# Performance work log

Measured on AMD Instinct MI355X. Metric: run time of the kernel, lower is better.

The kernel has to match this reference:

```python
import jax, jax.numpy as jnp
import numpy as np
import math

B, G, QLEN, KVLEN = 2, 2, 1024, 1024
DIN = 1024
NUM_HEADS = 16
QK_CH = 1024
V_CH = 1024
OUT_CH = 1024


def setup_inputs() -> dict:
    key = jax.random.key(0)
    ks = jax.random.split(key, 8)
    s_q = (1.0 / math.sqrt(DIN)) * math.sqrt(2.0)  # kaiming-ish scale
    inputs_q = jax.random.normal(ks[0], (B, G, QLEN, DIN), dtype=jnp.float32)
    inputs_kv = jax.random.normal(ks[1], (B, G, KVLEN, DIN), dtype=jnp.float32)
    Wq = jax.random.normal(ks[2], (QK_CH, DIN), dtype=jnp.float32) * s_q
    bq = jnp.zeros((QK_CH,), dtype=jnp.float32)
    Wk = jax.random.normal(ks[3], (QK_CH, DIN), dtype=jnp.float32) * s_q
    bk = jnp.zeros((QK_CH,), dtype=jnp.float32)
    Wv = jax.random.normal(ks[4], (V_CH, DIN), dtype=jnp.float32) * s_q
    bv = jnp.zeros((V_CH,), dtype=jnp.float32)
    Wo = jax.random.normal(ks[5], (OUT_CH, V_CH), dtype=jnp.float32) * (1.0 / math.sqrt(V_CH)) * math.sqrt(2.0)
    bo = jnp.zeros((OUT_CH,), dtype=jnp.float32)
    return {"inputs_q": inputs_q, "inputs_kv": inputs_kv,
            "Wq": Wq, "bq": bq, "Wk": Wk, "bk": bk,
            "Wv": Wv, "bv": bv, "Wo": Wo, "bo": bo}


def reference(inputs_q, inputs_kv, Wq, bq, Wk, bk, Wv, bv, Wo, bo):
    h = NUM_HEADS
    qk_per_head = QK_CH // h
    v_per_head = V_CH // h
    b, g, n, _ = inputs_q.shape
    m = inputs_kv.shape[2]
    # linear projections (torch Linear: x @ W.T + b)
    q = inputs_q @ Wq.T + bq          # [b,g,n,qk]
    k = inputs_kv @ Wk.T + bk         # [b,g,m,qk]
    v = inputs_kv @ Wv.T + bv         # [b,g,m,vc]
    q = q.reshape(b, g, n, h, qk_per_head)
    k = k.reshape(b, g, m, h, qk_per_head)
    v = v.reshape(b, g, m, h, v_per_head)
    scale = 1.0 / math.sqrt(qk_per_head)
    attn_scores = jnp.einsum('bgnhc,bgmhc->bghnm', q, k) * scale
    attn_probs = jax.nn.softmax(attn_scores, axis=-1)  # dropout_prob=0 -> identity
    result = jnp.einsum('bghnm,bgmhd->bgnhd', attn_probs, v)
    result = result.reshape(b, g, n, h * v_per_head)
    out = result @ Wo.T + bo
    return (out, attn_probs)
```

## Files before the change

kernel.cpp:

```cpp
#include <hip/hip_runtime.h>
#include <math.h>

#define DIN   1024
#define NH    16
#define HD    64
#define SEQ   1024
#define BG    4
#define MROWS (BG*SEQ)

typedef unsigned short u16;
typedef __attribute__((ext_vector_type(8))) short bf16x8;
typedef __attribute__((ext_vector_type(4))) float f32x4;

__device__ __forceinline__ u16 f2bf(float f) {
    unsigned u = __float_as_uint(f);
    u += 0x7fff + ((u >> 16) & 1);
    return (u16)(u >> 16);
}

__global__ __launch_bounds__(256)
void convert_bf(const float* __restrict__ a, u16* __restrict__ o)
{
    const size_t i = ((size_t)blockIdx.x * 256 + threadIdx.x) * 4;
    const float4 v = *(const float4*)(a + i);
    ushort4 r;
    r.x = f2bf(v.x); r.y = f2bf(v.y); r.z = f2bf(v.z); r.w = f2bf(v.w);
    *(ushort4*)(o + i) = r;
}

template<int OUT_BF16>
__global__ __launch_bounds__(256)
void gemm_bt(const u16* __restrict__ A, int lda,
             const u16* __restrict__ W, int ldw,
             const float* __restrict__ bias,
             void* __restrict__ Cout, int ldc, int K)
{
    __shared__ u16 As[128][40];
    __shared__ u16 Ws[128][40];
    const int tid = threadIdx.x;
    const int wave = tid >> 6, lane = tid & 63;
    const int wm = wave >> 1, wn = wave & 1;
    const int q = lane >> 4, c = lane & 15;
    const int row0 = blockIdx.y * 128, col0 = blockIdx.x * 128;
    const int rs = tid >> 2, kg = (tid & 3) * 8;

    f32x4 acc[4][4];
    #pragma unroll
    for (int i = 0; i < 4; i++)
        #pragma unroll
        for (int j = 0; j < 4; j++) acc[i][j] = (f32x4){0.f, 0.f, 0.f, 0.f};

    for (int k0 = 0; k0 < K; k0 += 32) {
        *(float4*)&As[rs][kg]      = *(const float4*)(A + (size_t)(row0 + rs) * lda + k0 + kg);
        *(float4*)&As[rs + 64][kg] = *(const float4*)(A + (size_t)(row0 + rs + 64) * lda + k0 + kg);
        *(float4*)&Ws[rs][kg]      = *(const float4*)(W + (size_t)(col0 + rs) * ldw + k0 + kg);
        *(float4*)&Ws[rs + 64][kg] = *(const float4*)(W + (size_t)(col0 + rs + 64) * ldw + k0 + kg);
        __syncthreads();
        bf16x8 af[4], bfr[4];
        #pragma unroll
        for (int i = 0; i < 4; i++) af[i]  = *(const bf16x8*)&As[wm * 64 + i * 16 + c][q * 8];
        #pragma unroll
        for (int j = 0; j < 4; j++) bfr[j] = *(const bf16x8*)&Ws[wn * 64 + j * 16 + c][q * 8];
        #pragma unroll
        for (int i = 0; i < 4; i++)
            #pragma unroll
            for (int j = 0; j < 4; j++)
                acc[i][j] = __builtin_amdgcn_mfma_f32_16x16x32_bf16(af[i], bfr[j], acc[i][j], 0, 0, 0);
        __syncthreads();
    }

    float bv[4];
    #pragma unroll
    for (int j = 0; j < 4; j++) bv[j] = bias[col0 + wn * 64 + j * 16 + c];
    #pragma unroll
    for (int i = 0; i < 4; i++)
        #pragma unroll
        for (int r = 0; r < 4; r++) {
            const size_t row = row0 + wm * 64 + i * 16 + q * 4 + r;
            #pragma unroll
            for (int j = 0; j < 4; j++) {
                const int col = col0 + wn * 64 + j * 16 + c;
                const float v = acc[i][j][r] + bv[j];
                if (OUT_BF16) ((u16*)Cout)[row * ldc + col] = f2bf(v);
                else          ((float*)Cout)[row * ldc + col] = v;
            }
        }
}

__global__ __launch_bounds__(256, 2)
void attn_fused(const u16* __restrict__ Qbf, const u16* __restrict__ Kbf,
                const u16* __restrict__ Vbf, float* __restrict__ P,
                u16* __restrict__ Rbf)
{
    __shared__ u16 Ps[4][128][40];
    __shared__ u16 Vs[4][64][40];
    __shared__ float red[128][2];

    const int tid = threadIdx.x;
    const int wave = tid >> 6, lane = tid & 63;
    const int wm = wave >> 1, wn = wave & 1;
    const int q = lane >> 4, c = lane & 15;

    const int lin = blockIdx.y * 8 + blockIdx.x;
    const int xcd = lin & 7, li = lin >> 3;
    const int bgh = (xcd << 3) | (li >> 3);
    const int n0  = (li & 7) * 128;

    const int bg = bgh >> 4, h = bgh & 15;
    const u16* Qh = Qbf + (size_t)bg * SEQ * DIN + h * HD;
    const u16* Kh = Kbf + (size_t)bg * SEQ * DIN + h * HD;
    const u16* Vh = Vbf + (size_t)bg * SEQ * DIN + h * HD;
    float* Ph = P + (size_t)bgh * SEQ * SEQ;

    bf16x8 qf[4][2];
    #pragma unroll
    for (int i = 0; i < 4; i++)
        #pragma unroll
        for (int ks = 0; ks < 2; ks++)
            qf[i][ks] = *(const bf16x8*)(Qh + (size_t)(n0 + wm * 64 + i * 16 + c) * DIN + ks * 32 + q * 8);

    float lsum[4][4];
    #pragma unroll
    for (int i = 0; i < 4; i++)
        #pragma unroll
        for (int r = 0; r < 4; r++) lsum[i][r] = 0.f;

    #pragma unroll 1
    for (int m0 = 0; m0 < SEQ; m0 += 128) {
        f32x4 acc[4][4];
        #pragma unroll
        for (int i = 0; i < 4; i++)
            #pragma unroll
            for (int j = 0; j < 4; j++) acc[i][j] = (f32x4){0.f, 0.f, 0.f, 0.f};
        #pragma unroll
        for (int ks = 0; ks < 2; ks++) {
            bf16x8 kf[4];
            #pragma unroll
            for (int j = 0; j < 4; j++)
                kf[j] = *(const bf16x8*)(Kh + (size_t)(m0 + wn * 64 + j * 16 + c) * DIN + ks * 32 + q * 8);
            #pragma unroll
            for (int i = 0; i < 4; i++)
                #pragma unroll
                for (int j = 0; j < 4; j++)
                    acc[i][j] = __builtin_amdgcn_mfma_f32_16x16x32_bf16(qf[i][ks], kf[j], acc[i][j], 0, 0, 0);
        }
        #pragma unroll
        for (int i = 0; i < 4; i++)
            #pragma unroll
            for (int r = 0; r < 4; r++) {
                #pragma unroll
                for (int j = 0; j < 4; j++)
                    lsum[i][r] += __expf(acc[i][j][r] * 0.125f);
            }
    }

    #pragma unroll
    for (int i = 0; i < 4; i++)
        #pragma unroll
        for (int r = 0; r < 4; r++) {
            float s = lsum[i][r];
            s += __shfl_xor(s, 1);
            s += __shfl_xor(s, 2);
            s += __shfl_xor(s, 4);
            s += __shfl_xor(s, 8);
            if (c == 0) red[wm * 64 + i * 16 + q * 4 + r][wn] = s;
        }
    __syncthreads();
    float invl[4][4];
    #pragma unroll
    for (int i = 0; i < 4; i++)
        #pragma unroll
        for (int r = 0; r < 4; r++) {
            const int rl = wm * 64 + i * 16 + q * 4 + r;
            invl[i][r] = 1.f / (red[rl][0] + red[rl][1]);
        }

    f32x4 oacc[4][2];
    #pragma unroll
    for (int i = 0; i < 4; i++) {
        oacc[i][0] = (f32x4){0.f, 0.f, 0.f, 0.f};
        oacc[i][1] = (f32x4){0.f, 0.f, 0.f, 0.f};
    }

    #pragma unroll 1
    for (int m0 = 0; m0 < SEQ; m0 += 128) {
        f32x4 acc[4][4];
        #pragma unroll
        for (int i = 0; i < 4; i++)
            #pragma unroll
            for (int j = 0; j < 4; j++) acc[i][j] = (f32x4){0.f, 0.f, 0.f, 0.f};
        #pragma unroll
        for (int ks = 0; ks < 2; ks++) {
            bf16x8 kf[4];
            #pragma unroll
            for (int j = 0; j < 4; j++)
                kf[j] = *(const bf16x8*)(Kh + (size_t)(m0 + wn * 64 + j * 16 + c) * DIN + ks * 32 + q * 8);
            #pragma unroll
            for (int i = 0; i < 4; i++)
                #pragma unroll
                for (int j = 0; j < 4; j++)
                    acc[i][j] = __builtin_amdgcn_mfma_f32_16x16x32_bf16(qf[i][ks], kf[j], acc[i][j], 0, 0, 0);
        }

        #pragma unroll
        for (int it = 0; it < 4; it++) {
            const int mv = it * 32 + (tid >> 3);
            const int dg = (tid & 7) * 8;
            const bf16x8 vv = *(const bf16x8*)(Vh + (size_t)(m0 + mv) * DIN + dg);
            const u16* vp = (const u16*)&vv;
            #pragma unroll
            for (int u = 0; u < 8; u++) Vs[it][dg + u][tid >> 3] = vp[u];
        }

        #pragma unroll
        for (int i = 0; i < 4; i++)
            #pragma unroll
            for (int j = 0; j < 4; j++) {
                const int ml = wn * 64 + j * 16 + c;
                const int mc = ml >> 5, mw = ml & 31;
                #pragma unroll
                for (int r = 0; r < 4; r++) {
                    const float p = __expf(acc[i][j][r] * 0.125f) * invl[i][r];
                    const int row = wm * 64 + i * 16 + q * 4 + r;
                    Ph[(size_t)(n0 + row) * SEQ + m0 + ml] = p;
                    Ps[mc][row][mw] = f2bf(p);
                }
            }
        __syncthreads();

        #pragma unroll
        for (int ks = 0; ks < 4; ks++) {
            bf16x8 pf[4], vf[2];
            #pragma unroll
            for (int i = 0; i < 4; i++) pf[i] = *(const bf16x8*)&Ps[ks][wm * 64 + i * 16 + c][q * 8];
            #pragma unroll
            for (int j = 0; j < 2; j++) vf[j] = *(const bf16x8*)&Vs[ks][wn * 32 + j * 16 + c][q * 8];
            #pragma unroll
            for (int i = 0; i < 4; i++)
                #pragma unroll
                for (int j = 0; j < 2; j++)
                    oacc[i][j] = __builtin_amdgcn_mfma_f32_16x16x32_bf16(pf[i], vf[j], oacc[i][j], 0, 0, 0);
        }
        __syncthreads();
    }

    #pragma unroll
    for (int i = 0; i < 4; i++)
        #pragma unroll
        for (int r = 0; r < 4; r++) {
            const size_t row = (size_t)bg * SEQ + n0 + wm * 64 + i * 16 + q * 4 + r;
            #pragma unroll
            for (int j = 0; j < 2; j++) {
                const int d = wn * 32 + j * 16 + c;
                Rbf[row * DIN + h * HD + d] = f2bf(oacc[i][j][r]);
            }
        }
}

extern "C" void kernel_launch(void* const* d_in, const int* in_sizes, int n_in,
                              void* d_out, int out_size, void* d_ws, size_t ws_size,
                              hipStream_t stream)
{
    const float* xq  = (const float*)d_in[0];
    const float* xkv = (const float*)d_in[1];
    const float* Wq  = (const float*)d_in[2];
    const float* bq  = (const float*)d_in[3];
    const float* Wk  = (const float*)d_in[4];
    const float* bk  = (const float*)d_in[5];
    const float* Wv  = (const float*)d_in[6];
    const float* bv  = (const float*)d_in[7];
    const float* Wo  = (const float*)d_in[8];
    const float* bo  = (const float*)d_in[9];

    float* out0 = (float*)d_out;
    float* out1 = out0 + (size_t)MROWS * DIN;

    u16* xq_bf  = (u16*)d_ws;
    u16* xkv_bf = xq_bf  + (size_t)MROWS * DIN;
    u16* Wq_bf  = xkv_bf + (size_t)MROWS * DIN;
    u16* Wk_bf  = Wq_bf  + (size_t)DIN * DIN;
    u16* Wv_bf  = Wk_bf  + (size_t)DIN * DIN;
    u16* Wo_bf  = Wv_bf  + (size_t)DIN * DIN;
    u16* Qbf    = Wo_bf  + (size_t)DIN * DIN;
    u16* Kbf    = Qbf    + (size_t)MROWS * DIN;
    u16* Vbf    = Kbf    + (size_t)MROWS * DIN;
    u16* Rbf    = Vbf    + (size_t)MROWS * DIN;

    const dim3 blk(256);

    convert_bf<<<dim3(4096), blk, 0, stream>>>(xq,  xq_bf);
    convert_bf<<<dim3(4096), blk, 0, stream>>>(xkv, xkv_bf);
    convert_bf<<<dim3(1024), blk, 0, stream>>>(Wq,  Wq_bf);
    convert_bf<<<dim3(1024), blk, 0, stream>>>(Wk,  Wk_bf);
    convert_bf<<<dim3(1024), blk, 0, stream>>>(Wv,  Wv_bf);
    convert_bf<<<dim3(1024), blk, 0, stream>>>(Wo,  Wo_bf);

    gemm_bt<1><<<dim3(8, 32), blk, 0, stream>>>(xq_bf,  DIN, Wq_bf, DIN, bq, Qbf, DIN, DIN);
    gemm_bt<1><<<dim3(8, 32), blk, 0, stream>>>(xkv_bf, DIN, Wk_bf, DIN, bk, Kbf, DIN, DIN);
    gemm_bt<1><<<dim3(8, 32), blk, 0, stream>>>(xkv_bf, DIN, Wv_bf, DIN, bv, Vbf, DIN, DIN);

    attn_fused<<<dim3(8, 64), blk, 0, stream>>>(Qbf, Kbf, Vbf, out1, Rbf);

    gemm_bt<0><<<dim3(8, 32), blk, 0, stream>>>(Rbf, DIN, Wo_bf, DIN, bo, out0, DIN, DIN);
}
```

Before: 483.2 us.

## Fuse fp32-to-bf16 conversion into GEMM loads and produce transposed V directly

Drops the six separate fp32-to-bf16 conversion kernels. The GEMMs now read fp32 inputs and weights directly and convert them while staging into LDS. The V projection is computed as Wv·xkvᵀ so it writes V already transposed, with a row-wise bias. The attention kernel then reads V fragments straight from global memory, with no LDS transpose, and processes the score tile in two halves to lower register pressure, so occupancy can be raised to 3 blocks. The cost is that the GEMMs move twice the input bytes as fp32 and re-convert tiles they load more than once, and the V reads in the PV step become uncached global loads.

```diff
diff --git a/kernel.cpp b/kernel.cpp
--- a/kernel.cpp
+++ b/kernel.cpp
@@ -18,20 +18,26 @@
     return (u16)(u >> 16);
 }
 
+template<int FP32>
+__device__ __forceinline__ void stage8(u16* dst, const void* __restrict__ src, size_t off)
+{
+    if (FP32) {
+        const float* p = (const float*)src + off;
+        const float4 a = *(const float4*)p;
+        const float4 b = *(const float4*)(p + 4);
+        ushort4 r0, r1;
+        r0.x = f2bf(a.x); r0.y = f2bf(a.y); r0.z = f2bf(a.z); r0.w = f2bf(a.w);
+        r1.x = f2bf(b.x); r1.y = f2bf(b.y); r1.z = f2bf(b.z); r1.w = f2bf(b.w);
+        *(ushort4*)dst = r0; *(ushort4*)(dst + 4) = r1;
+    } else {
+        *(float4*)dst = *(const float4*)((const u16*)src + off);
+    }
+}
+
+template<int A_FP32, int W_FP32, int OUT_BF16, int BIAS_ROW>
 __global__ __launch_bounds__(256)
-void convert_bf(const float* __restrict__ a, u16* __restrict__ o)
-{
-    const size_t i = ((size_t)blockIdx.x * 256 + threadIdx.x) * 4;
-    const float4 v = *(const float4*)(a + i);
-    ushort4 r;
-    r.x = f2bf(v.x); r.y = f2bf(v.y); r.z = f2bf(v.z); r.w = f2bf(v.w);
-    *(ushort4*)(o + i) = r;
-}
-
-template<int OUT_BF16>
-__global__ __launch_bounds__(256)
-void gemm_bt(const u16* __restrict__ A, int lda,
-             const u16* __restrict__ W, int ldw,
+void gemm_bt(const void* __restrict__ A, int lda,
+             const void* __restrict__ W, int ldw,
              const float* __restrict__ bias,
              void* __restrict__ Cout, int ldc, int K)
 {
@@ -51,10 +57,10 @@
         for (int j = 0; j < 4; j++) acc[i][j] = (f32x4){0.f, 0.f, 0.f, 0.f};
 
     for (int k0 = 0; k0 < K; k0 += 32) {
-        *(float4*)&As[rs][kg]      = *(const float4*)(A + (size_t)(row0 + rs) * lda + k0 + kg);
-        *(float4*)&As[rs + 64][kg] = *(const float4*)(A + (size_t)(row0 + rs + 64) * lda + k0 + kg);
-        *(float4*)&Ws[rs][kg]      = *(const float4*)(W + (size_t)(col0 + rs) * ldw + k0 + kg);
-        *(float4*)&Ws[rs + 64][kg] = *(const float4*)(W + (size_t)(col0 + rs + 64) * ldw + k0 + kg);
+        stage8<A_FP32>(&As[rs][kg],      A, (size_t)(row0 + rs) * lda + k0 + kg);
+        stage8<A_FP32>(&As[rs + 64][kg], A, (size_t)(row0 + rs + 64) * lda + k0 + kg);
+        stage8<W_FP32>(&Ws[rs][kg],      W, (size_t)(col0 + rs) * ldw + k0 + kg);
+        stage8<W_FP32>(&Ws[rs + 64][kg], W, (size_t)(col0 + rs + 64) * ldw + k0 + kg);
         __syncthreads();
         bf16x8 af[4], bfr[4];
         #pragma unroll
@@ -69,9 +75,16 @@
         __syncthreads();
     }
 
-    float bv[4];
-    #pragma unroll
-    for (int j = 0; j < 4; j++) bv[j] = bias[col0 + wn * 64 + j * 16 + c];
+    float bcol[4], brow[4][4];
+    if (!BIAS_ROW) {
+        #pragma unroll
+        for (int j = 0; j < 4; j++) bcol[j] = bias[col0 + wn * 64 + j * 16 + c];
+    } else {
+        #pragma unroll
+        for (int i = 0; i < 4; i++)
+            #pragma unroll
+            for (int r = 0; r < 4; r++) brow[i][r] = bias[row0 + wm * 64 + i * 16 + q * 4 + r];
+    }
     #pragma unroll
     for (int i = 0; i < 4; i++)
         #pragma unroll
@@ -80,20 +93,19 @@
             #pragma unroll
             for (int j = 0; j < 4; j++) {
                 const int col = col0 + wn * 64 + j * 16 + c;
-                const float v = acc[i][j][r] + bv[j];
+                const float v = acc[i][j][r] + (BIAS_ROW ? brow[i][r] : bcol[j]);
                 if (OUT_BF16) ((u16*)Cout)[row * ldc + col] = f2bf(v);
                 else          ((float*)Cout)[row * ldc + col] = v;
             }
         }
 }
 
-__global__ __launch_bounds__(256, 2)
+__global__ __launch_bounds__(256, 3)
 void attn_fused(const u16* __restrict__ Qbf, const u16* __restrict__ Kbf,
-                const u16* __restrict__ Vbf, float* __restrict__ P,
+                const u16* __restrict__ Vt, float* __restrict__ P,
                 u16* __restrict__ Rbf)
 {
-    __shared__ u16 Ps[4][128][40];
-    __shared__ u16 Vs[4][64][40];
+    __shared__ u16 Ps[4][128][36];
     __shared__ float red[128][2];
 
     const int tid = threadIdx.x;
@@ -109,7 +121,7 @@
     const int bg = bgh >> 4, h = bgh & 15;
     const u16* Qh = Qbf + (size_t)bg * SEQ * DIN + h * HD;
     const u16* Kh = Kbf + (size_t)bg * SEQ * DIN + h * HD;
-    const u16* Vh = Vbf + (size_t)bg * SEQ * DIN + h * HD;
+    const u16* Vh = Vt  + (size_t)(h * HD) * MROWS + bg * SEQ;
     float* Ph = P + (size_t)bgh * SEQ * SEQ;
 
     bf16x8 qf[4][2];
@@ -184,48 +196,39 @@
 
     #pragma unroll 1
     for (int m0 = 0; m0 < SEQ; m0 += 128) {
-        f32x4 acc[4][4];
-        #pragma unroll
-        for (int i = 0; i < 4; i++)
-            #pragma unroll
-            for (int j = 0; j < 4; j++) acc[i][j] = (f32x4){0.f, 0.f, 0.f, 0.f};
-        #pragma unroll
-        for (int ks = 0; ks < 2; ks++) {
-            bf16x8 kf[4];
-            #pragma unroll
-            for (int j = 0; j < 4; j++)
-                kf[j] = *(const bf16x8*)(Kh + (size_t)(m0 + wn * 64 + j * 16 + c) * DIN + ks * 32 + q * 8);
+        #pragma unroll 1
+        for (int half = 0; half < 2; half++) {
+            f32x4 acc[4][2];
+            #pragma unroll
+            for (int i = 0; i < 4; i++) { acc[i][0] = (f32x4){0.f,0.f,0.f,0.f}; acc[i][1] = (f32x4){0.f,0.f,0.f,0.f}; }
+            #pragma unroll
+            for (int ks = 0; ks < 2; ks++) {
+                bf16x8 kf[2];
+                #pragma unroll
+                for (int j = 0; j < 2; j++)
+                    kf[j] = *(const bf16x8*)(Kh + (size_t)(m0 + wn * 64 + half * 32 + j * 16 + c) * DIN + ks * 32 + q * 8);
+                #pragma unroll
+                for (int i = 0; i < 4; i++)
+                    #pragma unroll
+                    for (int j = 0; j < 2; j++)
+                        acc[i][j] = __builtin_amdgcn_mfma_f32_16x16x32_bf16(qf[i][ks], kf[j], acc[i][j], 0, 0, 0);
+            }
+            const int mc = wn * 2 + half;
             #pragma unroll
             for (int i = 0; i < 4; i++)
                 #pragma unroll
-                for (int j = 0; j < 4; j++)
-                    acc[i][j] = __builtin_amdgcn_mfma_f32_16x16x32_bf16(qf[i][ks], kf[j], acc[i][j], 0, 0, 0);
-        }
-
-        #pragma unroll
-        for (int it = 0; it < 4; it++) {
-            const int mv = it * 32 + (tid >> 3);
-            const int dg = (tid & 7) * 8;
-            const bf16x8 vv = *(const bf16x8*)(Vh + (size_t)(m0 + mv) * DIN + dg);
-            const u16* vp = (const u16*)&vv;
-            #pragma unroll
-            for (int u = 0; u < 8; u++) Vs[it][dg + u][tid >> 3] = vp[u];
-        }
-
-        #pragma unroll
-        for (int i = 0; i < 4; i++)
-            #pragma unroll
-            for (int j = 0; j < 4; j++) {
-                const int ml = wn * 64 + j * 16 + c;
-                const int mc = ml >> 5, mw = ml & 31;
-                #pragma unroll
-                for (int r = 0; r < 4; r++) {
-                    const float p = __expf(acc[i][j][r] * 0.125f) * invl[i][r];
-                    const int row = wm * 64 + i * 16 + q * 4 + r;
-                    Ph[(size_t)(n0 + row) * SEQ + m0 + ml] = p;
-                    Ps[mc][row][mw] = f2bf(p);
+                for (int j = 0; j < 2; j++) {
+                    const int mw = j * 16 + c;
+                    const int ml = wn * 64 + half * 32 + mw;
+                    #pragma unroll
+                    for (int r = 0; r < 4; r++) {
+                        const float p = __expf(acc[i][j][r] * 0.125f) * invl[i][r];
+                        const int row = wm * 64 + i * 16 + q * 4 + r;
+                        Ph[(size_t)(n0 + row) * SEQ + m0 + ml] = p;
+                        Ps[mc][row][mw] = f2bf(p);
+                    }
                 }
-            }
+        }
         __syncthreads();
 
         #pragma unroll
@@ -234,7 +237,8 @@
             #pragma unroll
             for (int i = 0; i < 4; i++) pf[i] = *(const bf16x8*)&Ps[ks][wm * 64 + i * 16 + c][q * 8];
             #pragma unroll
-            for (int j = 0; j < 2; j++) vf[j] = *(const bf16x8*)&Vs[ks][wn * 32 + j * 16 + c][q * 8];
+            for (int j = 0; j < 2; j++)
+                vf[j] = *(const bf16x8*)(Vh + (size_t)(wn * 32 + j * 16 + c) * MROWS + m0 + ks * 32 + q * 8);
             #pragma unroll
             for (int i = 0; i < 4; i++)
                 #pragma unroll
@@ -275,31 +279,18 @@
     float* out0 = (float*)d_out;
     float* out1 = out0 + (size_t)MROWS * DIN;
 
-    u16* xq_bf  = (u16*)d_ws;
-    u16* xkv_bf = xq_bf  + (size_t)MROWS * DIN;
-    u16* Wq_bf  = xkv_bf + (size_t)MROWS * DIN;
-    u16* Wk_bf  = Wq_bf  + (size_t)DIN * DIN;
-    u16* Wv_bf  = Wk_bf  + (size_t)DIN * DIN;
-    u16* Wo_bf  = Wv_bf  + (size_t)DIN * DIN;
-    u16* Qbf    = Wo_bf  + (size_t)DIN * DIN;
-    u16* Kbf    = Qbf    + (size_t)MROWS * DIN;
-    u16* Vbf    = Kbf    + (size_t)MROWS * DIN;
-    u16* Rbf    = Vbf    + (size_t)MROWS * DIN;
+    u16* Qbf = (u16*)d_ws;
+    u16* Kbf = Qbf + (size_t)MROWS * DIN;
+    u16* Vt  = Kbf + (size_t)MROWS * DIN;
+    u16* Rbf = Vt  + (size_t)DIN * MROWS;
 
     const dim3 blk(256);
 
-    convert_bf<<<dim3(4096), blk, 0, stream>>>(xq,  xq_bf);
-    convert_bf<<<dim3(4096), blk, 0, stream>>>(xkv, xkv_bf);
-    convert_bf<<<dim3(1024), blk, 0, stream>>>(Wq,  Wq_bf);
-    convert_bf<<<dim3(1024), blk, 0, stream>>>(Wk,  Wk_bf);
-    convert_bf<<<dim3(1024), blk, 0, stream>>>(Wv,  Wv_bf);
-    convert_bf<<<dim3(1024), blk, 0, stream>>>(Wo,  Wo_bf);
-
-    gemm_bt<1><<<dim3(8, 32), blk, 0, stream>>>(xq_bf,  DIN, Wq_bf, DIN, bq, Qbf, DIN, DIN);
-    gemm_bt<1><<<dim3(8, 32), blk, 0, stream>>>(xkv_bf, DIN, Wk_bf, DIN, bk, Kbf, DIN, DIN);
-    gemm_bt<1><<<dim3(8, 32), blk, 0, stream>>>(xkv_bf, DIN, Wv_bf, DIN, bv, Vbf, DIN, DIN);
-
-    attn_fused<<<dim3(8, 64), blk, 0, stream>>>(Qbf, Kbf, Vbf, out1, Rbf);
-
-    gemm_bt<0><<<dim3(8, 32), blk, 0, stream>>>(Rbf, DIN, Wo_bf, DIN, bo, out0, DIN, DIN);
-}
+    gemm_bt<1,1,1,0><<<dim3(8, 32), blk, 0, stream>>>(xq,  DIN, Wq,  DIN, bq, Qbf, DIN, DIN);
+    gemm_bt<1,1,1,0><<<dim3(8, 32), blk, 0, stream>>>(xkv, DIN, Wk,  DIN, bk, Kbf, DIN, DIN);
+    gemm_bt<1,1,1,1><<<dim3(32, 8), blk, 0, stream>>>(Wv,  DIN, xkv, DIN, bv, Vt, MROWS, DIN);
+
+    attn_fused<<<dim3(8, 64), blk, 0, stream>>>(Qbf, Kbf, Vt, out1, Rbf);
+
+    gemm_bt<0,1,0,0><<<dim3(8, 32), blk, 0, stream>>>(Rbf, DIN, Wo, DIN, bo, out0, DIN, DIN);
+}
```

New measurement: 571.5 us. 1.18x slower.

## Transpose QK^T MFMA operands so probability stores become row-contiguous vectors

Applied to the files above, without the earlier changes.

The attention kernel now computes S^T by passing K fragments as the A operand and Q fragments as B. Each lane then holds four consecutive key columns for one query row, so the fp32 probability matrix can be written with 16-byte vector stores and the bf16 P tile in LDS with 8-byte stores, instead of scattered scalar writes. The row-sum reduction changes to cross-quad shuffles, and the LDS padding for Ps and Vs is shrunk. The new padding strides may create LDS bank conflicts on the transposed V writes or the P reads.

```diff
diff --git a/kernel.cpp b/kernel.cpp
--- a/kernel.cpp
+++ b/kernel.cpp
@@ -92,8 +92,8 @@
                 const u16* __restrict__ Vbf, float* __restrict__ P,
                 u16* __restrict__ Rbf)
 {
-    __shared__ u16 Ps[4][128][40];
-    __shared__ u16 Vs[4][64][40];
+    __shared__ u16 Ps[4][128][36];
+    __shared__ u16 Vs[4][64][34];
     __shared__ float red[128][2];
 
     const int tid = threadIdx.x;
@@ -114,66 +114,57 @@
 
     bf16x8 qf[4][2];
     #pragma unroll
-    for (int i = 0; i < 4; i++)
+    for (int jn = 0; jn < 4; jn++)
         #pragma unroll
         for (int ks = 0; ks < 2; ks++)
-            qf[i][ks] = *(const bf16x8*)(Qh + (size_t)(n0 + wm * 64 + i * 16 + c) * DIN + ks * 32 + q * 8);
-
-    float lsum[4][4];
-    #pragma unroll
-    for (int i = 0; i < 4; i++)
-        #pragma unroll
-        for (int r = 0; r < 4; r++) lsum[i][r] = 0.f;
+            qf[jn][ks] = *(const bf16x8*)(Qh + (size_t)(n0 + wm * 64 + jn * 16 + c) * DIN + ks * 32 + q * 8);
+
+    float lsum[4];
+    #pragma unroll
+    for (int jn = 0; jn < 4; jn++) lsum[jn] = 0.f;
 
     #pragma unroll 1
     for (int m0 = 0; m0 < SEQ; m0 += 128) {
         f32x4 acc[4][4];
         #pragma unroll
-        for (int i = 0; i < 4; i++)
-            #pragma unroll
-            for (int j = 0; j < 4; j++) acc[i][j] = (f32x4){0.f, 0.f, 0.f, 0.f};
+        for (int im = 0; im < 4; im++)
+            #pragma unroll
+            for (int jn = 0; jn < 4; jn++) acc[im][jn] = (f32x4){0.f, 0.f, 0.f, 0.f};
         #pragma unroll
         for (int ks = 0; ks < 2; ks++) {
             bf16x8 kf[4];
             #pragma unroll
-            for (int j = 0; j < 4; j++)
-                kf[j] = *(const bf16x8*)(Kh + (size_t)(m0 + wn * 64 + j * 16 + c) * DIN + ks * 32 + q * 8);
-            #pragma unroll
-            for (int i = 0; i < 4; i++)
-                #pragma unroll
-                for (int j = 0; j < 4; j++)
-                    acc[i][j] = __builtin_amdgcn_mfma_f32_16x16x32_bf16(qf[i][ks], kf[j], acc[i][j], 0, 0, 0);
-        }
-        #pragma unroll
-        for (int i = 0; i < 4; i++)
-            #pragma unroll
-            for (int r = 0; r < 4; r++) {
-                #pragma unroll
-                for (int j = 0; j < 4; j++)
-                    lsum[i][r] += __expf(acc[i][j][r] * 0.125f);
-            }
-    }
-
-    #pragma unroll
-    for (int i = 0; i < 4; i++)
-        #pragma unroll
-        for (int r = 0; r < 4; r++) {
-            float s = lsum[i][r];
-            s += __shfl_xor(s, 1);
-            s += __shfl_xor(s, 2);
-            s += __shfl_xor(s, 4);
-            s += __shfl_xor(s, 8);
-            if (c == 0) red[wm * 64 + i * 16 + q * 4 + r][wn] = s;
-        }
+            for (int im = 0; im < 4; im++)
+                kf[im] = *(const bf16x8*)(Kh + (size_t)(m0 + wn * 64 + im * 16 + c) * DIN + ks * 32 + q * 8);
+            #pragma unroll
+            for (int im = 0; im < 4; im++)
+                #pragma unroll
+                for (int jn = 0; jn < 4; jn++)
+                    acc[im][jn] = __builtin_amdgcn_mfma_f32_16x16x32_bf16(kf[im], qf[jn][ks], acc[im][jn], 0, 0, 0);
+        }
+        #pragma unroll
+        for (int im = 0; im < 4; im++)
+            #pragma unroll
+            for (int jn = 0; jn < 4; jn++)
+                #pragma unroll
+                for (int r = 0; r < 4; r++)
+                    lsum[jn] += __expf(acc[im][jn][r] * 0.125f);
+    }
+
+    #pragma unroll
+    for (int jn = 0; jn < 4; jn++) {
+        float s = lsum[jn];
+        s += __shfl_xor(s, 16);
+        s += __shfl_xor(s, 32);
+        if (q == 0) red[wm * 64 + jn * 16 + c][wn] = s;
+    }
     __syncthreads();
-    float invl[4][4];
-    #pragma unroll
-    for (int i = 0; i < 4; i++)
-        #pragma unroll
-        for (int r = 0; r < 4; r++) {
-            const int rl = wm * 64 + i * 16 + q * 4 + r;
-            invl[i][r] = 1.f / (red[rl][0] + red[rl][1]);
-        }
+    float invl[4];
+    #pragma unroll
+    for (int jn = 0; jn < 4; jn++) {
+        const int rl = wm * 64 + jn * 16 + c;
+        invl[jn] = 1.f / (red[rl][0] + red[rl][1]);
+    }
 
     f32x4 oacc[4][2];
     #pragma unroll
@@ -186,45 +177,45 @@
     for (int m0 = 0; m0 < SEQ; m0 += 128) {
         f32x4 acc[4][4];
         #pragma unroll
-        for (int i = 0; i < 4; i++)
-            #pragma unroll
-            for (int j = 0; j < 4; j++) acc[i][j] = (f32x4){0.f, 0.f, 0.f, 0.f};
+        for (int im = 0; im < 4; im++)
+            #pragma unroll
+            for (int jn = 0; jn < 4; jn++) acc[im][jn] = (f32x4){0.f, 0.f, 0.f, 0.f};
         #pragma unroll
         for (int ks = 0; ks < 2; ks++) {
             bf16x8 kf[4];
             #pragma unroll
-            for (int j = 0; j < 4; j++)
-                kf[j] = *(const bf16x8*)(Kh + (size_t)(m0 + wn * 64 + j * 16 + c) * DIN + ks * 32 + q * 8);
-            #pragma unroll
-            for (int i = 0; i < 4; i++)
-                #pragma unroll
-                for (int j = 0; j < 4; j++)
-                    acc[i][j] = __builtin_amdgcn_mfma_f32_16x16x32_bf16(qf[i][ks], kf[j], acc[i][j], 0, 0, 0);
+            for (int im = 0; im < 4; im++)
+                kf[im] = *(const bf16x8*)(Kh + (size_t)(m0 + wn * 64 + im * 16 + c) * DIN + ks * 32 + q * 8);
+            #pragma unroll
+            for (int im = 0; im < 4; im++)
+                #pragma unroll
+                for (int jn = 0; jn < 4; jn++)
+                    acc[im][jn] = __builtin_amdgcn_mfma_f32_16x16x32_bf16(kf[im], qf[jn][ks], acc[im][jn], 0, 0, 0);
         }
 
         #pragma unroll
         for (int it = 0; it < 4; it++) {
             const int mv = it * 32 + (tid >> 3);
             const int dg = (tid & 7) * 8;
-            const bf16x8 vv = *(const bf16x8*)(Vh + (size_t)(m0 + mv) * DIN + dg);
+            const bf16x8 vv = *(const bf16x8*)(Vh + (size_t)(bg * 0 + m0 + mv) * DIN + dg);
             const u16* vp = (const u16*)&vv;
             #pragma unroll
             for (int u = 0; u < 8; u++) Vs[it][dg + u][tid >> 3] = vp[u];
         }
 
         #pragma unroll
-        for (int i = 0; i < 4; i++)
-            #pragma unroll
-            for (int j = 0; j < 4; j++) {
-                const int ml = wn * 64 + j * 16 + c;
-                const int mc = ml >> 5, mw = ml & 31;
-                #pragma unroll
-                for (int r = 0; r < 4; r++) {
-                    const float p = __expf(acc[i][j][r] * 0.125f) * invl[i][r];
-                    const int row = wm * 64 + i * 16 + q * 4 + r;
-                    Ph[(size_t)(n0 + row) * SEQ + m0 + ml] = p;
-                    Ps[mc][row][mw] = f2bf(p);
-                }
+        for (int im = 0; im < 4; im++)
+            #pragma unroll
+            for (int jn = 0; jn < 4; jn++) {
+                const int n  = wm * 64 + jn * 16 + c;
+                const int mloc = wn * 64 + im * 16 + q * 4;
+                f32x4 p4;
+                #pragma unroll
+                for (int r = 0; r < 4; r++) p4[r] = __expf(acc[im][jn][r] * 0.125f) * invl[jn];
+                *(f32x4*)&Ph[(size_t)(n0 + n) * SEQ + m0 + mloc] = p4;
+                ushort4 pb;
+                pb.x = f2bf(p4[0]); pb.y = f2bf(p4[1]); pb.z = f2bf(p4[2]); pb.w = f2bf(p4[3]);
+                *(ushort4*)&Ps[mloc >> 5][n][mloc & 31] = pb;
             }
         __syncthreads();
 
```

Result: slower. 509.7 us (+5.5%).
